# Performance work log

Measured on AMD Instinct MI355X. Metric: run time of the kernel, lower is better.

## Reference

```python
import jax, jax.numpy as jnp
import numpy as np

EPS = 1e-5

def conv1d(x, w, stride=2):
    # x: [N, Cin, L], w: [Cout, Cin, K], VALID padding
    return jax.lax.conv_general_dilated(x, w, (stride,), 'VALID',
                                         dimension_numbers=('NCH', 'OIH', 'NCH'))

def ln(x, g, b):
    # LayerNorm over last dim
    mu = jnp.mean(x, axis=-1, keepdims=True)
    var = jnp.mean((x - mu) ** 2, axis=-1, keepdims=True)
    return (x - mu) * jax.lax.rsqrt(var + EPS) * g + b

def block(x, w, g, b):
    return jax.nn.relu(ln(conv1d(x, w), g, b))

def setup_inputs() -> dict:
    key = jax.random.key(0)
    ks = jax.random.split(key, 20)
    B, CH, H, W = 4096, 143, 8, 8
    def p(k, shape, fan_in):
        return jax.random.normal(k, shape, dtype=jnp.float32) * (1.0 / np.sqrt(fan_in))
    inp = {
        'x': jax.random.normal(ks[0], (B, CH, H, W), dtype=jnp.float32),
        'w1': p(ks[1], (16, 2, 3), 6),
        'w2': p(ks[2], (28, 16, 3), 48),
        'w3': p(ks[3], (28, 28, 3), 84),
        'w4': p(ks[4], (28, 28, 3), 84),
        'f1': p(ks[5], (4, 2, 3), 6),
        'f2': p(ks[6], (4, 4, 3), 12),
        'f3': p(ks[7], (4, 4, 3), 12),
        'f4': p(ks[8], (4, 4, 3), 12),
        'ln1_w': jnp.ones((71,), jnp.float32), 'ln1_b': jnp.zeros((71,), jnp.float32),
        'ln2_w': jnp.ones((35,), jnp.float32), 'ln2_b': jnp.zeros((35,), jnp.float32),
        'ln3_w': jnp.ones((17,), jnp.float32), 'ln3_b': jnp.zeros((17,), jnp.float32),
        'ln4_w': jnp.ones((8,), jnp.float32), 'ln4_b': jnp.zeros((8,), jnp.float32),
    }
    return inp

def reference(x, w1, w2, w3, w4, f1, f2, f3, f4,
              ln1_w, ln1_b, ln2_w, ln2_b, ln3_w, ln3_b, ln4_w, ln4_b):
    b, ch, h, w = x.shape
    cr = x[:, :, 3:5, :]   # [b, ch, 2, w]
    cc = x[:, :, :, 3:5]   # [b, ch, h, 2]
    # FFT magnitude along spectral axis (axis=1)
    cr_fft = jnp.abs(jnp.fft.fft(cr, axis=1)).astype(jnp.float32)
    cc_fft = jnp.abs(jnp.fft.fft(cc, axis=1)).astype(jnp.float32)
    # reshape to [b*w (or b*h), 2, ch] sequences
    cr = jnp.transpose(cr, (0, 2, 3, 1)).reshape(b * w, 2, ch)
    cc = jnp.transpose(cc, (0, 2, 3, 1)).reshape(b * h, 2, ch)
    cr_fft = jnp.transpose(cr_fft, (0, 2, 3, 1)).reshape(b * w, 2, ch)
    cc_fft = jnp.transpose(cc_fft, (0, 2, 3, 1)).reshape(b * h, 2, ch)
    # spatial towers: 143 -> 71 -> 35 -> 17 -> 8, channels 2->16->28->28->28
    cr = block(cr, w1, ln1_w, ln1_b); cc = block(cc, w1, ln1_w, ln1_b)
    cr = block(cr, w2, ln2_w, ln2_b); cc = block(cc, w2, ln2_w, ln2_b)
    cr = block(cr, w3, ln3_w, ln3_b); cc = block(cc, w3, ln3_w, ln3_b)
    cr = block(cr, w4, ln4_w, ln4_b); cc = block(cc, w4, ln4_w, ln4_b)
    # fft towers: channels 2->4->4->4->4
    cr_fft = block(cr_fft, f1, ln1_w, ln1_b); cc_fft = block(cc_fft, f1, ln1_w, ln1_b)
    cr_fft = block(cr_fft, f2, ln2_w, ln2_b); cc_fft = block(cc_fft, f2, ln2_w, ln2_b)
    cr_fft = block(cr_fft, f3, ln3_w, ln3_b); cc_fft = block(cc_fft, f3, ln3_w, ln3_b)
    cr_fft = block(cr_fft, f4, ln4_w, ln4_b); cc_fft = block(cc_fft, f4, ln4_w, ln4_b)
    cr = jnp.transpose(cr.reshape(b, w, -1, 8), (0, 2, 1, 3))          # [b,28,w,8]
    cc = jnp.transpose(cc.reshape(b, h, -1, 8), (0, 2, 1, 3))          # [b,28,h,8]
    cr_fft = jnp.transpose(cr_fft.reshape(b, w, -1, 8), (0, 2, 1, 3))  # [b,4,w,8]
    cc_fft = jnp.transpose(cc_fft.reshape(b, h, -1, 8), (0, 2, 1, 3))  # [b,4,h,8]
    return jnp.concatenate([cr, cc, cr_fft, cc_fft], axis=1)           # [b,64,8,8]
```

## Files before the change

### kernel.cpp

```cpp
#include <hip/hip_runtime.h>
#include <math.h>

typedef _Float16 h16;
typedef _Float16 h16x2 __attribute__((ext_vector_type(2)));

#define NS 65536
#define VSTR 131072

__global__ __launch_bounds__(256) void k_gather(const float* __restrict__ x,
                                                float* __restrict__ xv,
                                                float* __restrict__ tw) {
  const int b = blockIdx.x;
  if (b < 4096) {
    const float* xb = x + (size_t)b * 9152;
    const int base = b * 32;
    for (int i = threadIdx.x; i < 9152; i += 256) {
      float v = xb[i];
      int c = i >> 6, pos = i & 63;
      if (pos >= 24 && pos < 40)
        xv[(size_t)c * VSTR + base + (pos - 24)] = v;
      int wc = pos & 7;
      if (wc == 3 || wc == 4)
        xv[(size_t)c * VSTR + base + 16 + ((pos >> 3) << 1) + (wc - 3)] = v;
    }
  } else {
    for (int i = threadIdx.x; i < 10296; i += 256) {
      int k = i / 143, n = i - k * 143;
      int e = (k * n) % 143;
      float ang = 6.2831853071795864769f * (float)e / 143.0f;
      float s, c;
      sincosf(ang, &s, &c);
      tw[2 * i] = c;
      tw[2 * i + 1] = s;
    }
  }
}

__global__ __launch_bounds__(256, 2) void k_dft(const float* __restrict__ xv,
                                                const float* __restrict__ tw,
                                                h16* __restrict__ fm) {
  const int v = blockIdx.x * 256 + threadIdx.x;
  float xr[143];
#pragma unroll
  for (int n = 0; n < 143; ++n) xr[n] = xv[(size_t)n * VSTR + v];

  for (int k = 0; k < 72; ++k) {
    const float* __restrict__ twk = tw + k * 286;
    float re = 0.f, im = 0.f;
#pragma unroll
    for (int n = 0; n < 143; ++n) {
      re = fmaf(xr[n], twk[2 * n], re);
      im = fmaf(xr[n], twk[2 * n + 1], im);
    }
    float m = sqrtf(re * re + im * im);
    fm[(size_t)k * VSTR + v] = (h16)m;
    if (k) fm[(size_t)(143 - k) * VSTR + v] = (h16)m;
  }
}

__device__ __forceinline__ void smap(int& d, int& w, int& va, int& vb,
                                     int& bi, int& u) {
  int lane = threadIdx.x & 63;
  w = __builtin_amdgcn_readfirstlane(threadIdx.x >> 6);
  d = (int)blockIdx.x * 64 + lane;
  bi = d >> 4;
  u = d & 15;
  va = (u < 8) ? bi * 32 + ((u >> 2) << 3) + ((u & 3) << 1)
               : bi * 32 + 16 + ((u & 7) << 1);
  vb = va + 1;
}

__global__ __launch_bounds__(256, 2) void k_c12(const float* __restrict__ xv,
                                                const h16* __restrict__ fm,
                                                const float* __restrict__ w1,
                                                const float* __restrict__ w2,
                                                const float* __restrict__ f1,
                                                const float* __restrict__ f2,
                                                const float* __restrict__ l1g,
                                                const float* __restrict__ l1b,
                                                h16* __restrict__ z2,
                                                float* __restrict__ s2) {
  __shared__ float red[4][32][64];
  const int lane = threadIdx.x & 63;
  const int w = threadIdx.x >> 6;
  const int d = (int)blockIdx.x * 64 + lane;
  const int bi = d >> 4, u = d & 15;
  const int va = (u < 8) ? bi * 32 + ((u >> 2) << 3) + ((u & 3) << 1)
                         : bi * 32 + 16 + ((u & 7) << 1);

  {
    float ps[20], pq[20];
#pragma unroll
    for (int j = 0; j < 20; ++j) { ps[j] = 0.f; pq[j] = 0.f; }
    const int ips = 18 * w;
    const int ipe = (ips + 18 < 71) ? (ips + 18) : 71;
    float2 r0 = *(const float2*)(xv + (size_t)(2 * ips) * VSTR + va);
    float A0 = r0.x, B0 = r0.y;
    h16x2 g0 = *(const h16x2*)(fm + (size_t)(2 * ips) * VSTR + va);
    float FA0 = (float)g0.x, FB0 = (float)g0.y;
#pragma unroll 1
    for (int ip = ips; ip < ipe; ++ip) {
      float2 r1 = *(const float2*)(xv + (size_t)(2 * ip + 1) * VSTR + va);
      float2 r2 = *(const float2*)(xv + (size_t)(2 * ip + 2) * VSTR + va);
      h16x2 g1 = *(const h16x2*)(fm + (size_t)(2 * ip + 1) * VSTR + va);
      h16x2 g2 = *(const h16x2*)(fm + (size_t)(2 * ip + 2) * VSTR + va);
#pragma unroll
      for (int c = 0; c < 16; ++c) {
        const float* wp = w1 + c * 6;
        float v = A0 * wp[0];
        v = fmaf(r1.x, wp[1], v); v = fmaf(r2.x, wp[2], v);
        v = fmaf(B0, wp[3], v); v = fmaf(r1.y, wp[4], v); v = fmaf(r2.y, wp[5], v);
        ps[c] += v; pq[c] = fmaf(v, v, pq[c]);
      }
      float FA1 = (float)g1.x, FB1 = (float)g1.y;
      float FA2 = (float)g2.x, FB2 = (float)g2.y;
#pragma unroll
      for (int c = 0; c < 4; ++c) {
        const float* wp = f1 + c * 6;
        float v = FA0 * wp[0];
        v = fmaf(FA1, wp[1], v); v = fmaf(FA2, wp[2], v);
        v = fmaf(FB0, wp[3], v); v = fmaf(FB1, wp[4], v); v = fmaf(FB2, wp[5], v);
        ps[16 + c] += v; pq[16 + c] = fmaf(v, v, pq[16 + c]);
      }
      A0 = r2.x; B0 = r2.y; FA0 = FA2; FB0 = FB2;
    }
#pragma unroll
    for (int j = 0; j < 20; ++j) red[w][j][lane] = ps[j];
    __syncthreads();
    float ts[5];
#pragma unroll
    for (int t = 0; t < 5; ++t) {
      int c = 5 * w + t;
      ts[t] = red[0][c][lane] + red[1][c][lane] + red[2][c][lane] + red[3][c][lane];
    }
    __syncthreads();
#pragma unroll
    for (int j = 0; j < 20; ++j) red[w][j][lane] = pq[j];
    __syncthreads();
    float tmu[5], tiv[5];
#pragma unroll
    for (int t = 0; t < 5; ++t) {
      int c = 5 * w + t;
      float tq = red[0][c][lane] + red[1][c][lane] + red[2][c][lane] + red[3][c][lane];
      float mu = ts[t] * (1.0f / 71.0f);
      float var = tq * (1.0f / 71.0f) - mu * mu;
      tmu[t] = mu; tiv[t] = rsqrtf(var + 1e-5f);
    }
    __syncthreads();
#pragma unroll
    for (int t = 0; t < 5; ++t) {
      int c = 5 * w + t;
      red[0][c][lane] = tmu[t];
      red[1][c][lane] = tiv[t];
    }
    __syncthreads();
  }

  const int ps2 = w * 9;
  const int pe2 = (ps2 + 9 < 35) ? (ps2 + 9) : 35;

  float sum[28], sq[28];
  float sums[4], sqs[4];

  {
    float mu1[16], inv1[16];
#pragma unroll
    for (int c = 0; c < 16; ++c) {
      mu1[c] = red[0][c][lane];
      inv1[c] = red[1][c][lane];
    }
#pragma unroll
    for (int j = 0; j < 28; ++j) { sum[j] = 0.f; sq[j] = 0.f; }

    float n0[16], n1[16], n2[16];
    float a2, b2, a3, b3, a4, b4, a5, b5, a6, b6;

    {
      float2 r0 = *(const float2*)(xv + (size_t)(4 * ps2) * VSTR + va);
      float2 r1 = *(const float2*)(xv + (size_t)(4 * ps2 + 1) * VSTR + va);
      float2 r2 = *(const float2*)(xv + (size_t)(4 * ps2 + 2) * VSTR + va);
      a2 = r2.x; b2 = r2.y;
      const float gg = l1g[2 * ps2], bb = l1b[2 * ps2];
#pragma unroll
      for (int c = 0; c < 16; ++c) {
        const float* wp = w1 + c * 6;
        float v = r0.x * wp[0];
        v = fmaf(r1.x, wp[1], v); v = fmaf(a2, wp[2], v);
        v = fmaf(r0.y, wp[3], v); v = fmaf(r1.y, wp[4], v); v = fmaf(b2, wp[5], v);
        n0[c] = fmaxf(fmaf((v - mu1[c]) * inv1[c], gg, bb), 0.f);
      }
      float2 r3 = *(const float2*)(xv + (size_t)(4 * ps2 + 3) * VSTR + va);
      float2 r4 = *(const float2*)(xv + (size_t)(4 * ps2 + 4) * VSTR + va);
      float2 r5 = *(const float2*)(xv + (size_t)(4 * ps2 + 5) * VSTR + va);
      float2 r6 = *(const float2*)(xv + (size_t)(4 * ps2 + 6) * VSTR + va);
      a3 = r3.x; b3 = r3.y; a4 = r4.x; b4 = r4.y;
      a5 = r5.x; b5 = r5.y; a6 = r6.x; b6 = r6.y;
    }

#pragma unroll 1
    for (int p = ps2; p < pe2; ++p) {
      {
        const float gg = l1g[2 * p + 1], bb = l1b[2 * p + 1];
#pragma unroll
        for (int c = 0; c < 16; ++c) {
          const float* wp = w1 + c * 6;
          float v = a2 * wp[0];
          v = fmaf(a3, wp[1], v); v = fmaf(a4, wp[2], v);
          v = fmaf(b2, wp[3], v); v = fmaf(b3, wp[4], v); v = fmaf(b4, wp[5], v);
          n1[c] = fmaxf(fmaf((v - mu1[c]) * inv1[c], gg, bb), 0.f);
        }
      }
      {
        const float gg = l1g[2 * p + 2], bb = l1b[2 * p + 2];
#pragma unroll
        for (int c = 0; c < 16; ++c) {
          const float* wp = w1 + c * 6;
          float v = a4 * wp[0];
          v = fmaf(a5, wp[1], v); v = fmaf(a6, wp[2], v);
          v = fmaf(b4, wp[3], v); v = fmaf(b5, wp[4], v); v = fmaf(b6, wp[5], v);
          n2[c] = fmaxf(fmaf((v - mu1[c]) * inv1[c], gg, bb), 0.f);
        }
      }
      a2 = a6; b2 = b6;
      {
        const int rbase = (p < 34) ? (4 * p + 7) : 139;
        const float* rp = xv + (size_t)rbase * VSTR + va;
        float2 r3 = *(const float2*)(rp);
        float2 r4 = *(const float2*)(rp + (size_t)VSTR);
        float2 r5 = *(const float2*)(rp + (size_t)2 * VSTR);
        float2 r6 = *(const float2*)(rp + (size_t)3 * VSTR);
        a3 = r3.x; b3 = r3.y; a4 = r4.x; b4 = r4.y;
        a5 = r5.x; b5 = r5.y; a6 = r6.x; b6 = r6.y;
      }
#pragma unroll
      for (int j = 0; j < 28; ++j) {
        const float* wp = w2 + j * 48;
        float acc = 0.f;
#pragma unroll
        for (int ci = 0; ci < 16; ++ci) {
          acc = fmaf(n0[ci], wp[ci * 3 + 0], acc);
          acc = fmaf(n1[ci], wp[ci * 3 + 1], acc);
          acc = fmaf(n2[ci], wp[ci * 3 + 2], acc);
        }
        z2[(size_t)(j * 35 + p) * NS + d] = (h16)acc;
        sum[j] += acc; sq[j] = fmaf(acc, acc, sq[j]);
      }
#pragma unroll
      for (int c = 0; c < 16; ++c) n0[c] = n2[c];
    }
  }

  {
    float mu1[4], inv1[4];
#pragma unroll
    for (int c = 0; c < 4; ++c) {
      mu1[c] = red[0][16 + c][lane];
      inv1[c] = red[1][16 + c][lane];
    }
#pragma unroll
    for (int c = 0; c < 4; ++c) { sums[c] = 0.f; sqs[c] = 0.f; }
    float n0[4], n1[4], n2[4];
    float a2, b2, a3, b3, a4, b4, a5, b5, a6, b6;

    {
      h16x2 r0 = *(const h16x2*)(fm + (size_t)(4 * ps2) * VSTR + va);
      h16x2 r1 = *(const h16x2*)(fm + (size_t)(4 * ps2 + 1) * VSTR + va);
      h16x2 r2 = *(const h16x2*)(fm + (size_t)(4 * ps2 + 2) * VSTR + va);
      float a0 = (float)r0.x, b0 = (float)r0.y;
      float a1 = (float)r1.x, b1 = (float)r1.y;
      a2 = (float)r2.x; b2 = (float)r2.y;
      const float gg = l1g[2 * ps2], bb = l1b[2 * ps2];
#pragma unroll
      for (int c = 0; c < 4; ++c) {
        const float* wp = f1 + c * 6;
        float v = a0 * wp[0];
        v = fmaf(a1, wp[1], v); v = fmaf(a2, wp[2], v);
        v = fmaf(b0, wp[3], v); v = fmaf(b1, wp[4], v); v = fmaf(b2, wp[5], v);
        n0[c] = fmaxf(fmaf((v - mu1[c]) * inv1[c], gg, bb), 0.f);
      }
      h16x2 r3 = *(const h16x2*)(fm + (size_t)(4 * ps2 + 3) * VSTR + va);
      h16x2 r4 = *(const h16x2*)(fm + (size_t)(4 * ps2 + 4) * VSTR + va);
      h16x2 r5 = *(const h16x2*)(fm + (size_t)(4 * ps2 + 5) * VSTR + va);
      h16x2 r6 = *(const h16x2*)(fm + (size_t)(4 * ps2 + 6) * VSTR + va);
      a3 = (float)r3.x; b3 = (float)r3.y; a4 = (float)r4.x; b4 = (float)r4.y;
      a5 = (float)r5.x; b5 = (float)r5.y; a6 = (float)r6.x; b6 = (float)r6.y;
    }

#pragma unroll 1
    for (int p = ps2; p < pe2; ++p) {
      {
        const float gg = l1g[2 * p + 1], bb = l1b[2 * p + 1];
#pragma unroll
        for (int c = 0; c < 4; ++c) {
          const float* wp = f1 + c * 6;
          float v = a2 * wp[0];
          v = fmaf(a3, wp[1], v); v = fmaf(a4, wp[2], v);
          v = fmaf(b2, wp[3], v); v = fmaf(b3, wp[4], v); v = fmaf(b4, wp[5], v);
          n1[c] = fmaxf(fmaf((v - mu1[c]) * inv1[c], gg, bb), 0.f);
        }
      }
      {
        const float gg = l1g[2 * p + 2], bb = l1b[2 * p + 2];
#pragma unroll
        for (int c = 0; c < 4; ++c) {
          const float* wp = f1 + c * 6;
          float v = a4 * wp[0];
          v = fmaf(a5, wp[1], v); v = fmaf(a6, wp[2], v);
          v = fmaf(b4, wp[3], v); v = fmaf(b5, wp[4], v); v = fmaf(b6, wp[5], v);
          n2[c] = fmaxf(fmaf((v - mu1[c]) * inv1[c], gg, bb), 0.f);
        }
      }
      a2 = a6; b2 = b6;
      {
        const int rbase = (p < 34) ? (4 * p + 7) : 139;
        const h16* rp = fm + (size_t)rbase * VSTR + va;
        h16x2 r3 = *(const h16x2*)(rp);
        h16x2 r4 = *(const h16x2*)(rp + (size_t)VSTR);
        h16x2 r5 = *(const h16x2*)(rp + (size_t)2 * VSTR);
        h16x2 r6 = *(const h16x2*)(rp + (size_t)3 * VSTR);
        a3 = (float)r3.x; b3 = (float)r3.y; a4 = (float)r4.x; b4 = (float)r4.y;
        a5 = (float)r5.x; b5 = (float)r5.y; a6 = (float)r6.x; b6 = (float)r6.y;
      }
#pragma unroll
      for (int co = 0; co < 4; ++co) {
        const float* wpo = f2 + co * 12;
        float acc = 0.f;
#pragma unroll
        for (int c = 0; c < 4; ++c) acc = fmaf(n0[c], wpo[c * 3 + 0], acc);
#pragma unroll
        for (int c = 0; c < 4; ++c) acc = fmaf(n1[c], wpo[c * 3 + 1], acc);
#pragma unroll
        for (int c = 0; c < 4; ++c) acc = fmaf(n2[c], wpo[c * 3 + 2], acc);
        z2[(size_t)(980 + co * 35 + p) * NS + d] = (h16)acc;
        sums[co] += acc; sqs[co] = fmaf(acc, acc, sqs[co]);
      }
#pragma unroll
      for (int c = 0; c < 4; ++c) n0[c] = n2[c];
    }
  }

  __syncthreads();
#pragma unroll
  for (int j = 0; j < 28; ++j) red[w][j][lane] = sum[j];
#pragma unroll
  for (int c = 0; c < 4; ++c) red[w][28 + c][lane] = sums[c];
  __syncthreads();
  const int jb = 7 * w;
  float fs[7], fq[7];
#pragma unroll
  for (int t = 0; t < 7; ++t)
    fs[t] = red[0][jb + t][lane] + red[1][jb + t][lane] +
            red[2][jb + t][lane] + red[3][jb + t][lane];
  float fss = red[0][28 + w][lane] + red[1][28 + w][lane] +
              red[2][28 + w][lane] + red[3][28 + w][lane];
  __syncthreads();
#pragma unroll
  for (int j = 0; j < 28; ++j) red[w][j][lane] = sq[j];
#pragma unroll
  for (int c = 0; c < 4; ++c) red[w][28 + c][lane] = sqs[c];
  __syncthreads();
#pragma unroll
  for (int t = 0; t < 7; ++t)
    fq[t] = red[0][jb + t][lane] + red[1][jb + t][lane] +
            red[2][jb + t][lane] + red[3][jb + t][lane];
  float fqs = red[0][28 + w][lane] + red[1][28 + w][lane] +
              red[2][28 + w][lane] + red[3][28 + w][lane];
#pragma unroll
  for (int t = 0; t < 7; ++t) {
    float mu = fs[t] * (1.0f / 35.0f);
    float var = fq[t] * (1.0f / 35.0f) - mu * mu;
    s2[(size_t)(jb + t) * NS + d] = mu;
    s2[(size_t)(28 + jb + t) * NS + d] = rsqrtf(var + 1e-5f);
  }
  {
    float mu = fss * (1.0f / 35.0f);
    float var = fqs * (1.0f / 35.0f) - mu * mu;
    s2[(size_t)(56 + w) * NS + d] = mu;
    s2[(size_t)(60 + w) * NS + d] = rsqrtf(var + 1e-5f);
  }
}

__global__ __launch_bounds__(256, 1) void k_c3(const h16* __restrict__ z2,
                                               const float* __restrict__ w3,
                                               const float* __restrict__ f3,
                                               const float* __restrict__ l2g,
                                               const float* __restrict__ l2b,
                                               const float* __restrict__ s2,
                                               h16* __restrict__ z3,
                                               float* __restrict__ s3) {
  int d, w, va, vb, bi, u;
  smap(d, w, va, vb, bi, u);

  {
    float acc[7][17];
#pragma unroll
    for (int j = 0; j < 7; ++j)
#pragma unroll
      for (int p = 0; p < 17; ++p) acc[j][p] = 0.f;
    const int cobase = 7 * w;
#pragma unroll 1
    for (int ci = 0; ci < 28; ++ci) {
      float mu = s2[(size_t)ci * NS + d];
      float inv = s2[(size_t)(28 + ci) * NS + d];
      float n[35];
#pragma unroll
      for (int t = 0; t < 35; ++t) {
        float raw = (float)z2[(size_t)(ci * 35 + t) * NS + d];
        n[t] = fmaxf(fmaf((raw - mu) * inv, l2g[t], l2b[t]), 0.f);
      }
#pragma unroll
      for (int j = 0; j < 7; ++j) {
        const float* wp = w3 + (cobase + j) * 84 + ci * 3;
        float w0 = wp[0], w1v = wp[1], w2v = wp[2];
#pragma unroll
        for (int p = 0; p < 17; ++p)
          acc[j][p] = fmaf(n[2 * p], w0,
                      fmaf(n[2 * p + 1], w1v,
                      fmaf(n[2 * p + 2], w2v, acc[j][p])));
      }
    }
#pragma unroll
    for (int j = 0; j < 7; ++j) {
      const int co = cobase + j;
      float sum = 0.f, sq = 0.f;
#pragma unroll
      for (int p = 0; p < 17; ++p) {
        sum += acc[j][p]; sq = fmaf(acc[j][p], acc[j][p], sq);
        z3[(size_t)(co * 17 + p) * NS + d] = (h16)acc[j][p];
      }
      float mu = sum * (1.0f / 17.0f);
      float var = sq * (1.0f / 17.0f) - mu * mu;
      s3[(size_t)co * NS + d] = mu;
      s3[(size_t)(28 + co) * NS + d] = rsqrtf(var + 1e-5f);
    }
  }
  {
    float acc[17];
#pragma unroll
    for (int p = 0; p < 17; ++p) acc[p] = 0.f;
    const int co = w;
#pragma unroll 1
    for (int ci = 0; ci < 4; ++ci) {
      float mu = s2[(size_t)(56 + ci) * NS + d];
      float inv = s2[(size_t)(60 + ci) * NS + d];
      float n[35];
#pragma unroll
      for (int t = 0; t < 35; ++t) {
        float raw = (float)z2[(size_t)(980 + ci * 35 + t) * NS + d];
        n[t] = fmaxf(fmaf((raw - mu) * inv, l2g[t], l2b[t]), 0.f);
      }
      const float* wp = f3 + co * 12 + ci * 3;
      float w0 = wp[0], w1v = wp[1], w2v = wp[2];
#pragma unroll
      for (int p = 0; p < 17; ++p)
        acc[p] = fmaf(n[2 * p], w0,
                 fmaf(n[2 * p + 1], w1v,
                 fmaf(n[2 * p + 2], w2v, acc[p])));
    }
    float sum = 0.f, sq = 0.f;
#pragma unroll
    for (int p = 0; p < 17; ++p) {
      sum += acc[p]; sq = fmaf(acc[p], acc[p], sq);
      z3[(size_t)(476 + co * 17 + p) * NS + d] = (h16)acc[p];
    }
    float mu = sum * (1.0f / 17.0f);
    float var = sq * (1.0f / 17.0f) - mu * mu;
    s3[(size_t)(56 + co) * NS + d] = mu;
    s3[(size_t)(60 + co) * NS + d] = rsqrtf(var + 1e-5f);
  }
}

__global__ __launch_bounds__(256, 1) void k_c4(const h16* __restrict__ z3,
                                               const float* __restrict__ w4,
                                               const float* __restrict__ f4,
                                               const float* __restrict__ l3g,
                                               const float* __restrict__ l3b,
                                               const float* __restrict__ l4g,
                                               const float* __restrict__ l4b,
                                               const float* __restrict__ s3,
                                               float* __restrict__ out) {
  int d, w, va, vb, bi, u;
  smap(d, w, va, vb, bi, u);

  {
    float acc[7][8];
#pragma unroll
    for (int j = 0; j < 7; ++j)
#pragma unroll
      for (int p = 0; p < 8; ++p) acc[j][p] = 0.f;
    const int cobase = 7 * w;
#pragma unroll 1
    for (int ci = 0; ci < 28; ++ci) {
      float mu = s3[(size_t)ci * NS + d];
      float inv = s3[(size_t)(28 + ci) * NS + d];
      float n[17];
#pragma unroll
      for (int t = 0; t < 17; ++t) {
        float raw = (float)z3[(size_t)(ci * 17 + t) * NS + d];
        n[t] = fmaxf(fmaf((raw - mu) * inv, l3g[t], l3b[t]), 0.f);
      }
#pragma unroll
      for (int j = 0; j < 7; ++j) {
        const float* wp = w4 + (cobase + j) * 84 + ci * 3;
        float w0 = wp[0], w1v = wp[1], w2v = wp[2];
#pragma unroll
        for (int p = 0; p < 8; ++p)
          acc[j][p] = fmaf(n[2 * p], w0,
                      fmaf(n[2 * p + 1], w1v,
                      fmaf(n[2 * p + 2], w2v, acc[j][p])));
      }
    }
#pragma unroll
    for (int j = 0; j < 7; ++j) {
      const int co = cobase + j;
      float sum = 0.f, sq = 0.f;
#pragma unroll
      for (int p = 0; p < 8; ++p) { sum += acc[j][p]; sq = fmaf(acc[j][p], acc[j][p], sq); }
      float mu = sum * 0.125f;
      float var = sq * 0.125f - mu * mu;
      float inv = rsqrtf(var + 1e-5f);
      const int ch = (u < 8) ? co : (28 + co);
      float* op = out + (size_t)bi * 4096 + (size_t)ch * 64 + (size_t)(u & 7) * 8;
      float o[8];
#pragma unroll
      for (int p = 0; p < 8; ++p)
        o[p] = fmaxf(fmaf((acc[j][p] - mu) * inv, l4g[p], l4b[p]), 0.f);
      *(float4*)(op) = make_float4(o[0], o[1], o[2], o[3]);
      *(float4*)(op + 4) = make_float4(o[4], o[5], o[6], o[7]);
    }
  }
  {
    float acc[8];
#pragma unroll
    for (int p = 0; p < 8; ++p) acc[p] = 0.f;
    const int co = w;
#pragma unroll 1
    for (int ci = 0; ci < 4; ++ci) {
      float mu = s3[(size_t)(56 + ci) * NS + d];
      float inv = s3[(size_t)(60 + ci) * NS + d];
      float n[17];
#pragma unroll
      for (int t = 0; t < 17; ++t) {
        float raw = (float)z3[(size_t)(476 + ci * 17 + t) * NS + d];
        n[t] = fmaxf(fmaf((raw - mu) * inv, l3g[t], l3b[t]), 0.f);
      }
      const float* wp = f4 + co * 12 + ci * 3;
      float w0 = wp[0], w1v = wp[1], w2v = wp[2];
#pragma unroll
      for (int p = 0; p < 8; ++p)
        acc[p] = fmaf(n[2 * p], w0,
                 fmaf(n[2 * p + 1], w1v,
                 fmaf(n[2 * p + 2], w2v, acc[p])));
    }
    float sum = 0.f, sq = 0.f;
#pragma unroll
    for (int p = 0; p < 8; ++p) { sum += acc[p]; sq = fmaf(acc[p], acc[p], sq); }
    float mu = sum * 0.125f;
    float var = sq * 0.125f - mu * mu;
    float inv = rsqrtf(var + 1e-5f);
    const int ch = (u < 8) ? (56 + co) : (60 + co);
    float* op = out + (size_t)bi * 4096 + (size_t)ch * 64 + (size_t)(u & 7) * 8;
    float o[8];
#pragma unroll
    for (int p = 0; p < 8; ++p)
      o[p] = fmaxf(fmaf((acc[p] - mu) * inv, l4g[p], l4b[p]), 0.f);
    *(float4*)(op) = make_float4(o[0], o[1], o[2], o[3]);
    *(float4*)(op + 4) = make_float4(o[4], o[5], o[6], o[7]);
  }
}

extern "C" void kernel_launch(void* const* d_in, const int* in_sizes, int n_in,
                              void* d_out, int out_size, void* d_ws, size_t ws_size,
                              hipStream_t stream) {
  const float* x   = (const float*)d_in[0];
  const float* w1  = (const float*)d_in[1];
  const float* w2  = (const float*)d_in[2];
  const float* w3  = (const float*)d_in[3];
  const float* w4  = (const float*)d_in[4];
  const float* f1  = (const float*)d_in[5];
  const float* f2  = (const float*)d_in[6];
  const float* f3  = (const float*)d_in[7];
  const float* f4  = (const float*)d_in[8];
  const float* l1g = (const float*)d_in[9];
  const float* l1b = (const float*)d_in[10];
  const float* l2g = (const float*)d_in[11];
  const float* l2b = (const float*)d_in[12];
  const float* l3g = (const float*)d_in[13];
  const float* l3b = (const float*)d_in[14];
  const float* l4g = (const float*)d_in[15];
  const float* l4b = (const float*)d_in[16];
  float* out = (float*)d_out;
  char* wsb = (char*)d_ws;

  float* xv = (float*)(wsb + 0);
  h16*   fm = (h16*)(wsb + 74973184ull);
  h16*   z2 = (h16*)(wsb + 112459776ull);
  h16*   z3 = (h16*)(wsb + 259260416ull);
  float* s2 = (float*)(wsb + 341049344ull);
  float* s3 = (float*)(wsb + 357826560ull);
  float* tw = (float*)(wsb + 374603776ull);

  k_gather<<<4097, 256, 0, stream>>>(x, xv, tw);
  k_dft<<<512, 256, 0, stream>>>(xv, tw, fm);
  k_c12<<<1024, 256, 0, stream>>>(xv, fm, w1, w2, f1, f2, l1g, l1b, z2, s2);
  k_c3<<<1024, 256, 0, stream>>>(z2, w3, f3, l2g, l2b, s2, z3, s3);
  k_c4<<<1024, 256, 0, stream>>>(z3, w4, f4, l3g, l3b, l4g, l4b, s3, out);
}
```

Baseline: 1.147 ms.

## Drop gather pass; read strided input directly in DFT and conv kernels

Removes the k_gather kernel that copied the center row/column slices of x into a channel-major buffer. k_dft and k_c12 now index the original [B,CH,8,8] input directly with per-thread offsets. Twiddle generation moves to its own small kernel, and rows are padded to 288 floats so the DFT can load twiddles as float4. This saves one full read of x plus the write and re-read of the gathered buffer, at the cost of less coalesced strided loads in the DFT and conv stages.

New measurement: 1.347 ms. 1.17x slower.

```diff
diff --git a/kernel.cpp b/kernel.cpp
--- a/kernel.cpp
+++ b/kernel.cpp
@@ -7,50 +7,47 @@
 #define NS 65536
 #define VSTR 131072
 
-__global__ __launch_bounds__(256) void k_gather(const float* __restrict__ x,
-                                                float* __restrict__ xv,
-                                                float* __restrict__ tw) {
-  const int b = blockIdx.x;
-  if (b < 4096) {
-    const float* xb = x + (size_t)b * 9152;
-    const int base = b * 32;
-    for (int i = threadIdx.x; i < 9152; i += 256) {
-      float v = xb[i];
-      int c = i >> 6, pos = i & 63;
-      if (pos >= 24 && pos < 40)
-        xv[(size_t)c * VSTR + base + (pos - 24)] = v;
-      int wc = pos & 7;
-      if (wc == 3 || wc == 4)
-        xv[(size_t)c * VSTR + base + 16 + ((pos >> 3) << 1) + (wc - 3)] = v;
-    }
-  } else {
-    for (int i = threadIdx.x; i < 10296; i += 256) {
-      int k = i / 143, n = i - k * 143;
-      int e = (k * n) % 143;
-      float ang = 6.2831853071795864769f * (float)e / 143.0f;
-      float s, c;
-      sincosf(ang, &s, &c);
-      tw[2 * i] = c;
-      tw[2 * i + 1] = s;
-    }
+
+__global__ __launch_bounds__(256) void k_tw(float* __restrict__ tw) {
+  int i = blockIdx.x * 256 + threadIdx.x;
+  if (i < 10296) {
+    int k = i / 143, n = i - k * 143;
+    int e = (k * n) % 143;
+    float ang = 6.2831853071795864769f * (float)e / 143.0f;
+    float s, c;
+    sincosf(ang, &s, &c);
+    tw[k * 288 + 2 * n] = c;
+    tw[k * 288 + 2 * n + 1] = s;
   }
 }
 
-__global__ __launch_bounds__(256, 2) void k_dft(const float* __restrict__ xv,
+__global__ __launch_bounds__(256, 2) void k_dft(const float* __restrict__ x,
                                                 const float* __restrict__ tw,
                                                 h16* __restrict__ fm) {
   const int v = blockIdx.x * 256 + threadIdx.x;
+  const int j = v & 31;
+  const int off = (j < 16) ? (24 + j)
+                           : ((((j - 16) >> 1) << 3) + 3 + ((j - 16) & 1));
+  const float* xb = x + (size_t)(v >> 5) * 9152 + off;
   float xr[143];
 #pragma unroll
-  for (int n = 0; n < 143; ++n) xr[n] = xv[(size_t)n * VSTR + v];
+  for (int n = 0; n < 143; ++n) xr[n] = xb[(size_t)n * 64];
 
   for (int k = 0; k < 72; ++k) {
-    const float* __restrict__ twk = tw + k * 286;
+    const float* __restrict__ twk = tw + k * 288;
     float re = 0.f, im = 0.f;
 #pragma unroll
-    for (int n = 0; n < 143; ++n) {
-      re = fmaf(xr[n], twk[2 * n], re);
-      im = fmaf(xr[n], twk[2 * n + 1], im);
+    for (int n = 0; n < 142; n += 2) {
+      float4 t = *(const float4*)(twk + 2 * n);
+      re = fmaf(xr[n], t.x, re);
+      im = fmaf(xr[n], t.y, im);
+      re = fmaf(xr[n + 1], t.z, re);
+      im = fmaf(xr[n + 1], t.w, im);
+    }
+    {
+      float2 t = *(const float2*)(twk + 284);
+      re = fmaf(xr[142], t.x, re);
+      im = fmaf(xr[142], t.y, im);
     }
     float m = sqrtf(re * re + im * im);
     fm[(size_t)k * VSTR + v] = (h16)m;
@@ -70,7 +67,7 @@
   vb = va + 1;
 }
 
-__global__ __launch_bounds__(256, 2) void k_c12(const float* __restrict__ xv,
+__global__ __launch_bounds__(256, 2) void k_c12(const float* __restrict__ x,
                                                 const h16* __restrict__ fm,
                                                 const float* __restrict__ w1,
                                                 const float* __restrict__ w2,
@@ -87,6 +84,9 @@
   const int bi = d >> 4, u = d & 15;
   const int va = (u < 8) ? bi * 32 + ((u >> 2) << 3) + ((u & 3) << 1)
                          : bi * 32 + 16 + ((u & 7) << 1);
+  const int offA = (u < 8) ? (24 + ((u >> 2) << 3) + ((u & 3) << 1))
+                           : (((u & 7) << 3) + 3);
+  const float* xb = x + (size_t)bi * 9152 + offA;
 
   {
     float ps[20], pq[20];
@@ -94,22 +94,21 @@
     for (int j = 0; j < 20; ++j) { ps[j] = 0.f; pq[j] = 0.f; }
     const int ips = 18 * w;
     const int ipe = (ips + 18 < 71) ? (ips + 18) : 71;
-    float2 r0 = *(const float2*)(xv + (size_t)(2 * ips) * VSTR + va);
-    float A0 = r0.x, B0 = r0.y;
+    float A0 = xb[(size_t)(2 * ips) * 64], B0 = xb[(size_t)(2 * ips) * 64 + 1];
     h16x2 g0 = *(const h16x2*)(fm + (size_t)(2 * ips) * VSTR + va);
     float FA0 = (float)g0.x, FB0 = (float)g0.y;
 #pragma unroll 1
     for (int ip = ips; ip < ipe; ++ip) {
-      float2 r1 = *(const float2*)(xv + (size_t)(2 * ip + 1) * VSTR + va);
-      float2 r2 = *(const float2*)(xv + (size_t)(2 * ip + 2) * VSTR + va);
+      float A1 = xb[(size_t)(2 * ip + 1) * 64], B1 = xb[(size_t)(2 * ip + 1) * 64 + 1];
+      float A2 = xb[(size_t)(2 * ip + 2) * 64], B2 = xb[(size_t)(2 * ip + 2) * 64 + 1];
       h16x2 g1 = *(const h16x2*)(fm + (size_t)(2 * ip + 1) * VSTR + va);
       h16x2 g2 = *(const h16x2*)(fm + (size_t)(2 * ip + 2) * VSTR + va);
 #pragma unroll
       for (int c = 0; c < 16; ++c) {
         const float* wp = w1 + c * 6;
         float v = A0 * wp[0];
-        v = fmaf(r1.x, wp[1], v); v = fmaf(r2.x, wp[2], v);
-        v = fmaf(B0, wp[3], v); v = fmaf(r1.y, wp[4], v); v = fmaf(r2.y, wp[5], v);
+        v = fmaf(A1, wp[1], v); v = fmaf(A2, wp[2], v);
+        v = fmaf(B0, wp[3], v); v = fmaf(B1, wp[4], v); v = fmaf(B2, wp[5], v);
         ps[c] += v; pq[c] = fmaf(v, v, pq[c]);
       }
       float FA1 = (float)g1.x, FB1 = (float)g1.y;
@@ -122,7 +121,7 @@
         v = fmaf(FB0, wp[3], v); v = fmaf(FB1, wp[4], v); v = fmaf(FB2, wp[5], v);
         ps[16 + c] += v; pq[16 + c] = fmaf(v, v, pq[16 + c]);
       }
-      A0 = r2.x; B0 = r2.y; FA0 = FA2; FB0 = FB2;
+      A0 = A2; B0 = B2; FA0 = FA2; FB0 = FB2;
     }
 #pragma unroll
     for (int j = 0; j < 20; ++j) red[w][j][lane] = ps[j];
@@ -176,25 +175,23 @@
     float a2, b2, a3, b3, a4, b4, a5, b5, a6, b6;
 
     {
-      float2 r0 = *(const float2*)(xv + (size_t)(4 * ps2) * VSTR + va);
-      float2 r1 = *(const float2*)(xv + (size_t)(4 * ps2 + 1) * VSTR + va);
-      float2 r2 = *(const float2*)(xv + (size_t)(4 * ps2 + 2) * VSTR + va);
-      a2 = r2.x; b2 = r2.y;
+      float a0 = xb[(size_t)(4 * ps2) * 64],     b0 = xb[(size_t)(4 * ps2) * 64 + 1];
+      float a1 = xb[(size_t)(4 * ps2 + 1) * 64], b1 = xb[(size_t)(4 * ps2 + 1) * 64 + 1];
+      a2 = xb[(size_t)(4 * ps2 + 2) * 64];       b2 = xb[(size_t)(4 * ps2 + 2) * 64 + 1];
       const float gg = l1g[2 * ps2], bb = l1b[2 * ps2];
 #pragma unroll
       for (int c = 0; c < 16; ++c) {
         const float* wp = w1 + c * 6;
-        float v = r0.x * wp[0];
-        v = fmaf(r1.x, wp[1], v); v = fmaf(a2, wp[2], v);
-        v = fmaf(r0.y, wp[3], v); v = fmaf(r1.y, wp[4], v); v = fmaf(b2, wp[5], v);
+        float v = a0 * wp[0];
+        v = fmaf(a1, wp[1], v); v = fmaf(a2, wp[2], v);
+        v = fmaf(b0, wp[3], v); v = fmaf(b1, wp[4], v); v = fmaf(b2, wp[5], v);
         n0[c] = fmaxf(fmaf((v - mu1[c]) * inv1[c], gg, bb), 0.f);
       }
-      float2 r3 = *(const float2*)(xv + (size_t)(4 * ps2 + 3) * VSTR + va);
-      float2 r4 = *(const float2*)(xv + (size_t)(4 * ps2 + 4) * VSTR + va);
-      float2 r5 = *(const float2*)(xv + (size_t)(4 * ps2 + 5) * VSTR + va);
-      float2 r6 = *(const float2*)(xv + (size_t)(4 * ps2 + 6) * VSTR + va);
-      a3 = r3.x; b3 = r3.y; a4 = r4.x; b4 = r4.y;
-      a5 = r5.x; b5 = r5.y; a6 = r6.x; b6 = r6.y;
+      const float* rp = xb + (size_t)(4 * ps2 + 3) * 64;
+      a3 = rp[0];   b3 = rp[1];
+      a4 = rp[64];  b4 = rp[65];
+      a5 = rp[128]; b5 = rp[129];
+      a6 = rp[192]; b6 = rp[193];
     }
 
 #pragma unroll 1
@@ -224,13 +221,11 @@
       a2 = a6; b2 = b6;
       {
         const int rbase = (p < 34) ? (4 * p + 7) : 139;
-        const float* rp = xv + (size_t)rbase * VSTR + va;
-        float2 r3 = *(const float2*)(rp);
-        float2 r4 = *(const float2*)(rp + (size_t)VSTR);
-        float2 r5 = *(const float2*)(rp + (size_t)2 * VSTR);
-        float2 r6 = *(const float2*)(rp + (size_t)3 * VSTR);
-        a3 = r3.x; b3 = r3.y; a4 = r4.x; b4 = r4.y;
-        a5 = r5.x; b5 = r5.y; a6 = r6.x; b6 = r6.y;
+        const float* rp = xb + (size_t)rbase * 64;
+        a3 = rp[0];   b3 = rp[1];
+        a4 = rp[64];  b4 = rp[65];
+        a5 = rp[128]; b5 = rp[129];
+        a6 = rp[192]; b6 = rp[193];
       }
 #pragma unroll
       for (int j = 0; j < 28; ++j) {
@@ -592,17 +587,16 @@
   float* out = (float*)d_out;
   char* wsb = (char*)d_ws;
 
-  float* xv = (float*)(wsb + 0);
   h16*   fm = (h16*)(wsb + 74973184ull);
   h16*   z2 = (h16*)(wsb + 112459776ull);
   h16*   z3 = (h16*)(wsb + 259260416ull);
+  float* tw = (float*)(wsb + 330563584ull);
   float* s2 = (float*)(wsb + 341049344ull);
   float* s3 = (float*)(wsb + 357826560ull);
-  float* tw = (float*)(wsb + 374603776ull);
-
-  k_gather<<<4097, 256, 0, stream>>>(x, xv, tw);
-  k_dft<<<512, 256, 0, stream>>>(xv, tw, fm);
-  k_c12<<<1024, 256, 0, stream>>>(xv, fm, w1, w2, f1, f2, l1g, l1b, z2, s2);
+
+  k_tw<<<41, 256, 0, stream>>>(tw);
+  k_dft<<<512, 256, 0, stream>>>(x, tw, fm);
+  k_c12<<<1024, 256, 0, stream>>>(x, fm, w1, w2, f1, f2, l1g, l1b, z2, s2);
   k_c3<<<1024, 256, 0, stream>>>(z2, w3, f3, l2g, l2b, s2, z3, s3);
   k_c4<<<1024, 256, 0, stream>>>(z3, w4, f4, l3g, l3b, l4g, l4b, s3, out);
 }
```
